# Optimization experiments

Hardware: AMD Instinct MI355X
Metric: run time of the kernel (lower is better)

The kernel has to match this reference:

```python
import jax, jax.numpy as jnp
import numpy as np

# ---- production-scale dims (see shape_source) ----
B, S = 256, 512            # batch, seq_len
HD, INTD = 512, 256        # hidden_dim, hidden_dim // dim_div
N_TEST, N_ITEM, N_TAG = 1500, 9454, 912
N_USER = 7442
GE_ROWS = N_USER + N_ITEM  # LightGCN table: users + items
N_CONT = 3


def _layer_norm(x, g, b, eps=1e-5):
    mu = jnp.mean(x, axis=-1, keepdims=True)
    var = jnp.var(x, axis=-1, keepdims=True)
    return (x - mu) * jax.lax.rsqrt(var + eps) * g + b


def setup_inputs() -> dict:
    key = jax.random.key(0)
    ks = jax.random.split(key, 14)
    f = lambda k, shp, s=0.02: jax.random.normal(k, shp, dtype=jnp.float32) * s
    return {
        # forward data args
        "cate_testId": jax.random.randint(ks[0], (B, S), 0, N_TEST),
        "cate_itemId": jax.random.randint(ks[1], (B, S), 0, N_ITEM),
        "cate_tag": jax.random.randint(ks[2], (B, S), 0, N_TAG),
        "cont_feats": jax.random.normal(ks[3], (B, S, N_CONT), dtype=jnp.float32),
        "interaction": jax.random.randint(ks[4], (B, S), 0, 3),
        # learned parameters
        "emb_interaction": f(ks[5], (3, INTD)),
        "emb_testId": f(ks[6], (N_TEST + 1, INTD)),
        "emb_itemId": f(ks[7], (N_ITEM + 1, INTD)),
        "emb_tag": f(ks[8], (N_TAG + 1, INTD)),
        "graph_table": f(ks[9], (GE_ROWS, HD)),           # pre-trained LightGCN embedding (np.load in torch)
        "graph_W": f(ks[10], (HD, INTD), 0.05),            # graph_linear (in, out) layout
        "graph_b": jnp.zeros((INTD,), jnp.float32),
        "comb_W": f(ks[11], (INTD * 5, HD // 2)),          # intd*(3 cate + 1 graph + interaction)
        "comb_b": jnp.zeros((HD // 2,), jnp.float32),
        "comb_g": jnp.ones((HD // 2,), jnp.float32),
        "comb_beta": jnp.zeros((HD // 2,), jnp.float32),
        "cont_W": f(ks[12], (N_CONT, HD // 2), 0.1),
        "cont_b": jnp.zeros((HD // 2,), jnp.float32),
        "cont_g": jnp.ones((HD // 2,), jnp.float32),
        "cont_beta": jnp.zeros((HD // 2,), jnp.float32),
    }


def reference(cate_testId, cate_itemId, cate_tag, cont_feats, interaction,
              emb_interaction, emb_testId, emb_itemId, emb_tag,
              graph_table, graph_W, graph_b,
              comb_W, comb_b, comb_g, comb_beta,
              cont_W, cont_b, cont_g, cont_beta):
    # categorical + interaction embedding lookups: [B,S,INTD] each
    e_int = emb_interaction[interaction]
    e_test = emb_testId[cate_testId]
    e_item = emb_itemId[cate_itemId]
    e_tag = emb_tag[cate_tag]
    # graph embedding path: fused gather (replaces the CPU python-loop gather)
    # indexes row (n_userID - 1 + value) of the LightGCN table, value from data[0]=testId
    g = graph_table[N_USER - 1 + cate_testId]          # [B,S,HD]
    g = g @ graph_W + graph_b                          # [B,S,INTD]
    embed = jnp.concatenate([e_int, e_test, e_item, e_tag, g], axis=-1)  # [B,S,5*INTD]
    cate = _layer_norm(embed @ comb_W + comb_b, comb_g, comb_beta)       # [B,S,HD//2]
    cont = _layer_norm(cont_feats @ cont_W + cont_b, cont_g, cont_beta)  # [B,S,HD//2]
    return jnp.concatenate([cate, cont], axis=-1)                        # [B,S,HD]
```

## Files before the change

### kernel.cpp

```cpp
#include <hip/hip_runtime.h>
#include <hip/hip_bf16.h>

#define NTOK   (256 * 512)
#define N_USER 7442

using bf16 = __hip_bfloat16;
typedef float f32x4 __attribute__((ext_vector_type(4)));

static __device__ __forceinline__ float4 ld4(const float* p) {
    return *reinterpret_cast<const float4*>(p);
}
static __device__ __forceinline__ float bfl(unsigned u) {
    union { unsigned u; float f; } c; c.u = u << 16; return c.f;
}
static __device__ __forceinline__ float bfh(unsigned u) {
    union { unsigned u; float f; } c; c.u = u & 0xFFFF0000u; return c.f;
}
static __device__ __forceinline__ void st_nt4(float* p, float x, float y, float z, float w) {
    f32x4 v; v.x = x; v.y = y; v.z = z; v.w = w;
    __builtin_nontemporal_store(v, reinterpret_cast<f32x4*>(p));
}
static __device__ __forceinline__ float rnd_bf(float x) {
    return __bfloat162float(__float2bfloat16(x));
}
static __device__ __forceinline__ void st_bf4(bf16* dst, float4 v) {
    union { bf16 h[4]; uint2 u; } pk;
    pk.h[0] = __float2bfloat16(v.x);
    pk.h[1] = __float2bfloat16(v.y);
    pk.h[2] = __float2bfloat16(v.z);
    pk.h[3] = __float2bfloat16(v.w);
    *reinterpret_cast<uint2*>(dst) = pk.u;
}

template <int CTRL, int ROW_MASK>
static __device__ __forceinline__ float dpp_add(float x) {
    const int sh = __builtin_amdgcn_update_dpp(0, __float_as_int(x), CTRL, ROW_MASK, 0xf, true);
    return x + __int_as_float(sh);
}
static __device__ __forceinline__ float wave_sum(float x) {
    x = dpp_add<0x111, 0xf>(x);
    x = dpp_add<0x112, 0xf>(x);
    x = dpp_add<0x114, 0xf>(x);
    x = dpp_add<0x118, 0xf>(x);
    x = dpp_add<0x142, 0xa>(x);
    x = dpp_add<0x143, 0xc>(x);
    return __int_as_float(__builtin_amdgcn_readlane(__float_as_int(x), 63));
}
static __device__ __forceinline__ float dot4(float4 a, float4 b) {
    return a.x * b.x + a.y * b.y + a.z * b.z + a.w * b.w;
}

#define RG  8
#define RSP 16
#define NB_TESTG 188
#define NB_ITEM  591
#define NB_TAG   58
#define NB_INT   1
#define NB_PC    (NB_TESTG + NB_ITEM + NB_TAG + NB_INT)
#define NB_CONT  2048
#define NB_A     (NB_PC + NB_CONT)

__global__ __launch_bounds__(256) void precompute_cont_kernel(
    const float* __restrict__ emb_int,  const float* __restrict__ emb_test,
    const float* __restrict__ emb_item, const float* __restrict__ emb_tag,
    const float* __restrict__ graph_tab, const float* __restrict__ graph_W,
    const float* __restrict__ graph_b,
    const float* __restrict__ comb_W,   const float* __restrict__ comb_b,
    const float* __restrict__ cont_feats,
    const float* __restrict__ cont_W,   const float* __restrict__ cont_b,
    const float* __restrict__ cont_g,   const float* __restrict__ cont_beta,
    bf16* __restrict__ Pint, bf16* __restrict__ Ptestg,
    bf16* __restrict__ Pitem, bf16* __restrict__ Ptag,
    float* __restrict__ Rint, float* __restrict__ Rtestg,
    float* __restrict__ Ritem, float* __restrict__ Rtag,
    float* __restrict__ out) {
    __shared__ float lds[4096];
    const int tid  = threadIdx.x;
    const int w    = tid >> 6;
    const int lane = tid & 63;
    const int c    = lane * 4;
    const int b    = blockIdx.x;

    if (b >= NB_PC) {
        const float4 w0  = ld4(cont_W + 0 * 256 + c);
        const float4 w1  = ld4(cont_W + 1 * 256 + c);
        const float4 w2  = ld4(cont_W + 2 * 256 + c);
        const float4 cb  = ld4(cont_b + c);
        const float4 g42 = ld4(cont_g + c);
        const float4 b42 = ld4(cont_beta + c);

        const float inv256 = 1.f / 256.f;
        const float M0  = wave_sum(w0.x + w0.y + w0.z + w0.w) * inv256;
        const float M1  = wave_sum(w1.x + w1.y + w1.z + w1.w) * inv256;
        const float M2  = wave_sum(w2.x + w2.y + w2.z + w2.w) * inv256;
        const float M3  = wave_sum(cb.x + cb.y + cb.z + cb.w) * inv256;
        const float P00 = wave_sum(dot4(w0, w0)) * inv256;
        const float P11 = wave_sum(dot4(w1, w1)) * inv256;
        const float P22 = wave_sum(dot4(w2, w2)) * inv256;
        const float P33 = wave_sum(dot4(cb, cb)) * inv256;
        const float P01 = wave_sum(dot4(w0, w1)) * inv256;
        const float P02 = wave_sum(dot4(w0, w2)) * inv256;
        const float P12 = wave_sum(dot4(w1, w2)) * inv256;
        const float P03 = wave_sum(dot4(w0, cb)) * inv256;
        const float P13 = wave_sum(dot4(w1, cb)) * inv256;
        const float P23 = wave_sum(dot4(w2, cb)) * inv256;

        const int wid = (b - NB_PC) * 4 + w;
        const int t0  = wid * 16;
        for (int k4 = 0; k4 < 4; ++k4) {
            const int tb = t0 + k4 * 4;
            const float4 cf0 = ld4(cont_feats + (size_t)tb * 3);
            const float4 cf1 = ld4(cont_feats + (size_t)tb * 3 + 4);
            const float4 cf2 = ld4(cont_feats + (size_t)tb * 3 + 8);
            const float cf[12] = {cf0.x, cf0.y, cf0.z, cf0.w,
                                  cf1.x, cf1.y, cf1.z, cf1.w,
                                  cf2.x, cf2.y, cf2.z, cf2.w};
            #pragma unroll
            for (int j = 0; j < 4; ++j) {
                const int t = tb + j;
                const float c0 = cf[j * 3 + 0];
                const float c1 = cf[j * 3 + 1];
                const float c2 = cf[j * 3 + 2];
                const float mu2 = c0 * M0 + c1 * M1 + c2 * M2 + M3;
                const float e2  = c0 * c0 * P00 + c1 * c1 * P11 + c2 * c2 * P22 + P33
                                + 2.f * (c0 * c1 * P01 + c0 * c2 * P02 + c1 * c2 * P12
                                       + c0 * P03 + c1 * P13 + c2 * P23);
                const float var2 = e2 - mu2 * mu2;
                const float inv2 = rsqrtf(var2 + 1e-5f);

                const float ux = c0 * w0.x + c1 * w1.x + c2 * w2.x + cb.x;
                const float uy = c0 * w0.y + c1 * w1.y + c2 * w2.y + cb.y;
                const float uz = c0 * w0.z + c1 * w1.z + c2 * w2.z + cb.z;
                const float uw = c0 * w0.w + c1 * w1.w + c2 * w2.w + cb.w;

                st_nt4(out + (size_t)t * 512 + 256 + c,
                       (ux - mu2) * inv2 * g42.x + b42.x,
                       (uy - mu2) * inv2 * g42.y + b42.y,
                       (uz - mu2) * inv2 * g42.z + b42.z,
                       (uw - mu2) * inv2 * g42.w + b42.w);
            }
        }
        return;
    }

    const float* W0 = comb_W;
    const float* W1 = comb_W + 256 * 256;
    const float* W2 = comb_W + 512 * 256;
    const float* W3 = comb_W + 768 * 256;
    const float* W4 = comb_W + 1024 * 256;

    if (b < NB_TESTG) {
        const int row0 = b * RG;
        const int nr   = min(RG, 1500 - row0);

        for (int i = tid; i < nr * 512; i += 256) {
            const int r = i >> 9, m = i & 511;
            lds[r * 512 + m] = graph_tab[(size_t)(N_USER - 1 + row0 + r) * 512 + m];
        }
        __syncthreads();

        float4 acc[2];
        acc[0] = float4{0.f, 0.f, 0.f, 0.f};
        acc[1] = float4{0.f, 0.f, 0.f, 0.f};
        for (int m = 0; m < 512; m += 4) {
            const float4 wv0 = ld4(graph_W + (m + 0) * 256 + c);
            const float4 wv1 = ld4(graph_W + (m + 1) * 256 + c);
            const float4 wv2 = ld4(graph_W + (m + 2) * 256 + c);
            const float4 wv3 = ld4(graph_W + (m + 3) * 256 + c);
            #pragma unroll
            for (int r = 0; r < 2; ++r) {
                const int rr = min(w * 2 + r, nr - 1);
                const float4 e = ld4(&lds[rr * 512 + m]);
                acc[r].x += e.x * wv0.x + e.y * wv1.x + e.z * wv2.x + e.w * wv3.x;
                acc[r].y += e.x * wv0.y + e.y * wv1.y + e.z * wv2.y + e.w * wv3.y;
                acc[r].z += e.x * wv0.z + e.y * wv1.z + e.z * wv2.z + e.w * wv3.z;
                acc[r].w += e.x * wv0.w + e.y * wv1.w + e.z * wv2.w + e.w * wv3.w;
            }
        }
        __syncthreads();

        #pragma unroll
        for (int r = 0; r < 2; ++r)
            *reinterpret_cast<float4*>(&lds[(w * 2 + r) * 256 + c]) = acc[r];
        for (int i = tid; i < nr * 256; i += 256) {
            const int r = i >> 8, m = i & 255;
            lds[2048 + r * 256 + m] = emb_test[(size_t)(row0 + r) * 256 + m];
        }
        __syncthreads();

        float4 acc2[2];
        float4 bacc = float4{0.f, 0.f, 0.f, 0.f};
        acc2[0] = float4{0.f, 0.f, 0.f, 0.f};
        acc2[1] = float4{0.f, 0.f, 0.f, 0.f};
        for (int m = 0; m < 256; m += 4) {
            const float4 w40 = ld4(W4 + (m + 0) * 256 + c);
            const float4 w41 = ld4(W4 + (m + 1) * 256 + c);
            const float4 w42 = ld4(W4 + (m + 2) * 256 + c);
            const float4 w43 = ld4(W4 + (m + 3) * 256 + c);
            const float4 w10 = ld4(W1 + (m + 0) * 256 + c);
            const float4 w11 = ld4(W1 + (m + 1) * 256 + c);
            const float4 w12 = ld4(W1 + (m + 2) * 256 + c);
            const float4 w13 = ld4(W1 + (m + 3) * 256 + c);
            const float gb0 = graph_b[m + 0], gb1 = graph_b[m + 1];
            const float gb2 = graph_b[m + 2], gb3 = graph_b[m + 3];
            bacc.x += gb0 * w40.x + gb1 * w41.x + gb2 * w42.x + gb3 * w43.x;
            bacc.y += gb0 * w40.y + gb1 * w41.y + gb2 * w42.y + gb3 * w43.y;
            bacc.z += gb0 * w40.z + gb1 * w41.z + gb2 * w42.z + gb3 * w43.z;
            bacc.w += gb0 * w40.w + gb1 * w41.w + gb2 * w42.w + gb3 * w43.w;
            #pragma unroll
            for (int r = 0; r < 2; ++r) {
                const int rr = min(w * 2 + r, nr - 1);
                const float4 tv = ld4(&lds[rr * 256 + m]);
                const float4 ev = ld4(&lds[2048 + rr * 256 + m]);
                acc2[r].x += tv.x * w40.x + tv.y * w41.x + tv.z * w42.x + tv.w * w43.x
                           + ev.x * w10.x + ev.y * w11.x + ev.z * w12.x + ev.w * w13.x;
                acc2[r].y += tv.x * w40.y + tv.y * w41.y + tv.z * w42.y + tv.w * w43.y
                           + ev.x * w10.y + ev.y * w11.y + ev.z * w12.y + ev.w * w13.y;
                acc2[r].z += tv.x * w40.z + tv.y * w41.z + tv.z * w42.z + tv.w * w43.z
                           + ev.x * w10.z + ev.y * w11.z + ev.z * w12.z + ev.w * w13.z;
                acc2[r].w += tv.x * w40.w + tv.y * w41.w + tv.z * w42.w + tv.w * w43.w
                           + ev.x * w10.w + ev.y * w11.w + ev.z * w12.w + ev.w * w13.w;
            }
        }
        const float4 cbv = ld4(comb_b + c);
        #pragma unroll
        for (int r = 0; r < 2; ++r) {
            const int row = w * 2 + r;
            float4 o;
            o.x = acc2[r].x + bacc.x + cbv.x;
            o.y = acc2[r].y + bacc.y + cbv.y;
            o.z = acc2[r].z + bacc.z + cbv.z;
            o.w = acc2[r].w + bacc.w + cbv.w;
            const float rs = wave_sum(rnd_bf(o.x) + rnd_bf(o.y) + rnd_bf(o.z) + rnd_bf(o.w));
            if (row < nr) {
                st_bf4(Ptestg + (size_t)(row0 + row) * 256 + c, o);
                if (lane == 0) Rtestg[row0 + row] = rs;
            }
        }
    } else {
        const float* E; const float* W; bf16* P; float* R; int row0, Rn;
        const int sb = b - NB_TESTG;
        if (sb < NB_ITEM)               { E = emb_item; W = W2; P = Pitem; R = Ritem; row0 = sb * RSP;             Rn = 9455; }
        else if (sb < NB_ITEM + NB_TAG) { E = emb_tag;  W = W3; P = Ptag;  R = Rtag;  row0 = (sb - NB_ITEM) * RSP; Rn = 913;  }
        else                            { E = emb_int;  W = W0; P = Pint;  R = Rint;  row0 = 0;                    Rn = 3;    }
        const int nr = min(RSP, Rn - row0);

        for (int i = tid; i < nr * 256; i += 256) {
            const int r = i >> 8, m = i & 255;
            lds[r * 256 + m] = E[(size_t)(row0 + r) * 256 + m];
        }
        __syncthreads();

        if (w * 4 < nr) {
            float4 acc[4];
            #pragma unroll
            for (int r = 0; r < 4; ++r) acc[r] = float4{0.f, 0.f, 0.f, 0.f};
            for (int m = 0; m < 256; m += 4) {
                const float4 wv0 = ld4(W + (m + 0) * 256 + c);
                const float4 wv1 = ld4(W + (m + 1) * 256 + c);
                const float4 wv2 = ld4(W + (m + 2) * 256 + c);
                const float4 wv3 = ld4(W + (m + 3) * 256 + c);
                #pragma unroll
                for (int r = 0; r < 4; ++r) {
                    const int rr = min(w * 4 + r, nr - 1);
                    const float4 e = ld4(&lds[rr * 256 + m]);
                    acc[r].x += e.x * wv0.x + e.y * wv1.x + e.z * wv2.x + e.w * wv3.x;
                    acc[r].y += e.x * wv0.y + e.y * wv1.y + e.z * wv2.y + e.w * wv3.y;
                    acc[r].z += e.x * wv0.z + e.y * wv1.z + e.z * wv2.z + e.w * wv3.z;
                    acc[r].w += e.x * wv0.w + e.y * wv1.w + e.z * wv2.w + e.w * wv3.w;
                }
            }
            #pragma unroll
            for (int r = 0; r < 4; ++r) {
                const int row = w * 4 + r;
                const float rs = wave_sum(rnd_bf(acc[r].x) + rnd_bf(acc[r].y) +
                                          rnd_bf(acc[r].z) + rnd_bf(acc[r].w));
                if (row < nr) {
                    st_bf4(P + (size_t)(row0 + row) * 256 + c, acc[r]);
                    if (lane == 0) R[row0 + row] = rs;
                }
            }
        }
    }
}

__global__ __launch_bounds__(256) void main_cate_kernel(
    const int* __restrict__ testId, const int* __restrict__ itemId,
    const int* __restrict__ tagId,  const int* __restrict__ inter,
    const bf16* __restrict__ Pint, const bf16* __restrict__ Ptestg,
    const bf16* __restrict__ Pitem, const bf16* __restrict__ Ptag,
    const float* __restrict__ Rint, const float* __restrict__ Rtestg,
    const float* __restrict__ Ritem, const float* __restrict__ Rtag,
    const float* __restrict__ comb_g, const float* __restrict__ comb_beta,
    float* __restrict__ out) {
    const int wid  = blockIdx.x * 4 + (threadIdx.x >> 6);
    const int lane = threadIdx.x & 63;
    const int c    = lane * 4;

    const float4 g4 = ld4(comb_g + c);
    const float4 b4 = ld4(comb_beta + c);
    const uint2 p0 = *reinterpret_cast<const uint2*>(Pint + 0 * 256 + c);
    const uint2 p1 = *reinterpret_cast<const uint2*>(Pint + 1 * 256 + c);
    const uint2 p2 = *reinterpret_cast<const uint2*>(Pint + 2 * 256 + c);
    const float ri0 = Rint[0], ri1 = Rint[1], ri2 = Rint[2];

    const int tb = wid * 4;
    const int4 tiv = *reinterpret_cast<const int4*>(testId + tb);
    const int4 iiv = *reinterpret_cast<const int4*>(itemId + tb);
    const int4 tgv = *reinterpret_cast<const int4*>(tagId  + tb);
    const int4 ivv = *reinterpret_cast<const int4*>(inter  + tb);
    const int tis[4] = {tiv.x, tiv.y, tiv.z, tiv.w};
    const int iis[4] = {iiv.x, iiv.y, iiv.z, iiv.w};
    const int tgs[4] = {tgv.x, tgv.y, tgv.z, tgv.w};
    const int ivs[4] = {ivv.x, ivv.y, ivv.z, ivv.w};

    uint2 gT[4], gI[4], gG[4];
    float sT[4], sI[4], sG[4];
    #pragma unroll
    for (int j = 0; j < 4; ++j) {
        gT[j] = *reinterpret_cast<const uint2*>(Ptestg + (size_t)tis[j] * 256 + c);
        gI[j] = *reinterpret_cast<const uint2*>(Pitem  + (size_t)iis[j] * 256 + c);
        gG[j] = *reinterpret_cast<const uint2*>(Ptag   + (size_t)tgs[j] * 256 + c);
        sT[j] = Rtestg[tis[j]];
        sI[j] = Ritem[iis[j]];
        sG[j] = Rtag[tgs[j]];
    }

    #pragma unroll
    for (int j = 0; j < 4; ++j) {
        const int t = tb + j;

        uint2 u0;
        u0.x = ivs[j] == 0 ? p0.x : (ivs[j] == 1 ? p1.x : p2.x);
        u0.y = ivs[j] == 0 ? p0.y : (ivs[j] == 1 ? p1.y : p2.y);
        const float sInt = ivs[j] == 0 ? ri0 : (ivs[j] == 1 ? ri1 : ri2);

        const float vx = bfl(u0.x) + bfl(gT[j].x) + bfl(gI[j].x) + bfl(gG[j].x);
        const float vy = bfh(u0.x) + bfh(gT[j].x) + bfh(gI[j].x) + bfh(gG[j].x);
        const float vz = bfl(u0.y) + bfl(gT[j].y) + bfl(gI[j].y) + bfl(gG[j].y);
        const float vw = bfh(u0.y) + bfh(gT[j].y) + bfh(gI[j].y) + bfh(gG[j].y);

        const float s   = sInt + sT[j] + sI[j] + sG[j];
        const float ss  = wave_sum(vx * vx + vy * vy + vz * vz + vw * vw);
        const float mu  = s * (1.f / 256.f);
        const float var = ss * (1.f / 256.f) - mu * mu;
        const float inv = rsqrtf(var + 1e-5f);

        st_nt4(out + (size_t)t * 512 + c,
               (vx - mu) * inv * g4.x + b4.x,
               (vy - mu) * inv * g4.y + b4.y,
               (vz - mu) * inv * g4.z + b4.z,
               (vw - mu) * inv * g4.w + b4.w);
    }
}

extern "C" void kernel_launch(void* const* d_in, const int* in_sizes, int n_in,
                              void* d_out, int out_size, void* d_ws, size_t ws_size,
                              hipStream_t stream) {
    const int*   testId     = (const int*)d_in[0];
    const int*   itemId     = (const int*)d_in[1];
    const int*   tagId      = (const int*)d_in[2];
    const float* cont_feats = (const float*)d_in[3];
    const int*   inter      = (const int*)d_in[4];
    const float* emb_int    = (const float*)d_in[5];
    const float* emb_test   = (const float*)d_in[6];
    const float* emb_item   = (const float*)d_in[7];
    const float* emb_tag    = (const float*)d_in[8];
    const float* graph_tab  = (const float*)d_in[9];
    const float* graph_W    = (const float*)d_in[10];
    const float* graph_b    = (const float*)d_in[11];
    const float* comb_W     = (const float*)d_in[12];
    const float* comb_b     = (const float*)d_in[13];
    const float* comb_g     = (const float*)d_in[14];
    const float* comb_beta  = (const float*)d_in[15];
    const float* cont_W     = (const float*)d_in[16];
    const float* cont_b     = (const float*)d_in[17];
    const float* cont_g     = (const float*)d_in[18];
    const float* cont_beta  = (const float*)d_in[19];
    float* out              = (float*)d_out;

    bf16* ws     = (bf16*)d_ws;
    bf16* Pitem  = ws;
    bf16* Ptestg = Pitem  + 9455 * 256;
    bf16* Ptag   = Ptestg + 1500 * 256;
    bf16* Pint   = Ptag   +  913 * 256;
    float* Ritem  = (float*)(Pint + 3 * 256);
    float* Rtestg = Ritem  + 9455;
    float* Rtag   = Rtestg + 1500;
    float* Rint   = Rtag   +  913;

    precompute_cont_kernel<<<NB_A, 256, 0, stream>>>(
        emb_int, emb_test, emb_item, emb_tag, graph_tab, graph_W, graph_b,
        comb_W, comb_b, cont_feats, cont_W, cont_b, cont_g, cont_beta,
        Pint, Ptestg, Pitem, Ptag,
        Rint, Rtestg, Ritem, Rtag, out);

    main_cate_kernel<<<NTOK / (4 * 4), 256, 0, stream>>>(
        testId, itemId, tagId, inter,
        Pint, Ptestg, Pitem, Ptag,
        Rint, Rtestg, Ritem, Rtag,
        comb_g, comb_beta, out);
}
```

Baseline: 109.9 us.

## Split precompute GEMV K-dimension across two waves with 128-thread blocks

Shrinks the precompute/cont kernel to 128-thread blocks (two waves) and doubles the number of cont blocks to keep the same token coverage. In the table-projection blocks, each wave now handles all rows but only half of the reduction dimension, and the partial sums are combined through LDS. The aim is to load each weight row once per block for all rows instead of once per wave, cutting redundant global weight traffic. The cost is more accumulator registers (up to 16 float4), extra LDS reduction passes and barriers, and a larger LDS footprint.

```diff
diff --git a/kernel.cpp b/kernel.cpp
--- a/kernel.cpp
+++ b/kernel.cpp
@@ -50,17 +50,15 @@
     return a.x * b.x + a.y * b.y + a.z * b.z + a.w * b.w;
 }
 
-#define RG  8
-#define RSP 16
 #define NB_TESTG 188
 #define NB_ITEM  591
 #define NB_TAG   58
 #define NB_INT   1
 #define NB_PC    (NB_TESTG + NB_ITEM + NB_TAG + NB_INT)
-#define NB_CONT  2048
+#define NB_CONT  4096
 #define NB_A     (NB_PC + NB_CONT)
 
-__global__ __launch_bounds__(256) void precompute_cont_kernel(
+__global__ __launch_bounds__(128) void precompute_cont_kernel(
     const float* __restrict__ emb_int,  const float* __restrict__ emb_test,
     const float* __restrict__ emb_item, const float* __restrict__ emb_tag,
     const float* __restrict__ graph_tab, const float* __restrict__ graph_W,
@@ -74,7 +72,7 @@
     float* __restrict__ Rint, float* __restrict__ Rtestg,
     float* __restrict__ Ritem, float* __restrict__ Rtag,
     float* __restrict__ out) {
-    __shared__ float lds[4096];
+    __shared__ float lds[6400];
     const int tid  = threadIdx.x;
     const int w    = tid >> 6;
     const int lane = tid & 63;
@@ -105,7 +103,7 @@
         const float P13 = wave_sum(dot4(w1, cb)) * inv256;
         const float P23 = wave_sum(dot4(w2, cb)) * inv256;
 
-        const int wid = (b - NB_PC) * 4 + w;
+        const int wid = (b - NB_PC) * 2 + w;
         const int t0  = wid * 16;
         for (int k4 = 0; k4 < 4; ++k4) {
             const int tb = t0 + k4 * 4;
@@ -125,8 +123,7 @@
                 const float e2  = c0 * c0 * P00 + c1 * c1 * P11 + c2 * c2 * P22 + P33
                                 + 2.f * (c0 * c1 * P01 + c0 * c2 * P02 + c1 * c2 * P12
                                        + c0 * P03 + c1 * P13 + c2 * P23);
-                const float var2 = e2 - mu2 * mu2;
-                const float inv2 = rsqrtf(var2 + 1e-5f);
+                const float inv2 = rsqrtf(e2 - mu2 * mu2 + 1e-5f);
 
                 const float ux = c0 * w0.x + c1 * w1.x + c2 * w2.x + cb.x;
                 const float uy = c0 * w0.y + c1 * w1.y + c2 * w2.y + cb.y;
@@ -150,27 +147,28 @@
     const float* W4 = comb_W + 1024 * 256;
 
     if (b < NB_TESTG) {
-        const int row0 = b * RG;
-        const int nr   = min(RG, 1500 - row0);
-
-        for (int i = tid; i < nr * 512; i += 256) {
-            const int r = i >> 9, m = i & 511;
-            lds[r * 512 + m] = graph_tab[(size_t)(N_USER - 1 + row0 + r) * 512 + m];
-        }
-        __syncthreads();
-
-        float4 acc[2];
-        acc[0] = float4{0.f, 0.f, 0.f, 0.f};
-        acc[1] = float4{0.f, 0.f, 0.f, 0.f};
-        for (int m = 0; m < 512; m += 4) {
+        const int row0 = b * 8;
+        const int nr   = min(8, 1500 - row0);
+
+        for (int i = tid; i < 1024; i += 128) {
+            const int r = i >> 7, m4 = (i & 127) * 4;
+            const int rr = min(r, nr - 1);
+            *reinterpret_cast<float4*>(&lds[r * 512 + m4]) =
+                ld4(graph_tab + (size_t)(N_USER - 1 + row0 + rr) * 512 + m4);
+        }
+        __syncthreads();
+
+        float4 acc[8];
+        #pragma unroll
+        for (int r = 0; r < 8; ++r) acc[r] = float4{0.f, 0.f, 0.f, 0.f};
+        for (int m = w * 256; m < w * 256 + 256; m += 4) {
             const float4 wv0 = ld4(graph_W + (m + 0) * 256 + c);
             const float4 wv1 = ld4(graph_W + (m + 1) * 256 + c);
             const float4 wv2 = ld4(graph_W + (m + 2) * 256 + c);
             const float4 wv3 = ld4(graph_W + (m + 3) * 256 + c);
             #pragma unroll
-            for (int r = 0; r < 2; ++r) {
-                const int rr = min(w * 2 + r, nr - 1);
-                const float4 e = ld4(&lds[rr * 512 + m]);
+            for (int r = 0; r < 8; ++r) {
+                const float4 e = ld4(&lds[r * 512 + m]);
                 acc[r].x += e.x * wv0.x + e.y * wv1.x + e.z * wv2.x + e.w * wv3.x;
                 acc[r].y += e.x * wv0.y + e.y * wv1.y + e.z * wv2.y + e.w * wv3.y;
                 acc[r].z += e.x * wv0.z + e.y * wv1.z + e.z * wv2.z + e.w * wv3.z;
@@ -179,20 +177,33 @@
         }
         __syncthreads();
 
+        if (w == 0) {
+            #pragma unroll
+            for (int r = 0; r < 8; ++r)
+                *reinterpret_cast<float4*>(&lds[4096 + r * 256 + c]) = acc[r];
+        }
+        __syncthreads();
+        if (w == 1) {
+            #pragma unroll
+            for (int r = 0; r < 8; ++r) {
+                float4 t = ld4(&lds[4096 + r * 256 + c]);
+                t.x += acc[r].x; t.y += acc[r].y; t.z += acc[r].z; t.w += acc[r].w;
+                *reinterpret_cast<float4*>(&lds[4096 + r * 256 + c]) = t;
+            }
+        }
+        for (int i = tid; i < 512; i += 128) {
+            const int r = i >> 6, m4 = (i & 63) * 4;
+            const int rr = min(r, nr - 1);
+            *reinterpret_cast<float4*>(&lds[r * 256 + m4]) =
+                ld4(emb_test + (size_t)(row0 + rr) * 256 + m4);
+        }
+        __syncthreads();
+
+        float4 acc2[8];
+        float4 bacc = float4{0.f, 0.f, 0.f, 0.f};
         #pragma unroll
-        for (int r = 0; r < 2; ++r)
-            *reinterpret_cast<float4*>(&lds[(w * 2 + r) * 256 + c]) = acc[r];
-        for (int i = tid; i < nr * 256; i += 256) {
-            const int r = i >> 8, m = i & 255;
-            lds[2048 + r * 256 + m] = emb_test[(size_t)(row0 + r) * 256 + m];
-        }
-        __syncthreads();
-
-        float4 acc2[2];
-        float4 bacc = float4{0.f, 0.f, 0.f, 0.f};
-        acc2[0] = float4{0.f, 0.f, 0.f, 0.f};
-        acc2[1] = float4{0.f, 0.f, 0.f, 0.f};
-        for (int m = 0; m < 256; m += 4) {
+        for (int r = 0; r < 8; ++r) acc2[r] = float4{0.f, 0.f, 0.f, 0.f};
+        for (int m = w * 128; m < w * 128 + 128; m += 4) {
             const float4 w40 = ld4(W4 + (m + 0) * 256 + c);
             const float4 w41 = ld4(W4 + (m + 1) * 256 + c);
             const float4 w42 = ld4(W4 + (m + 2) * 256 + c);
@@ -208,10 +219,9 @@
             bacc.z += gb0 * w40.z + gb1 * w41.z + gb2 * w42.z + gb3 * w43.z;
             bacc.w += gb0 * w40.w + gb1 * w41.w + gb2 * w42.w + gb3 * w43.w;
             #pragma unroll
-            for (int r = 0; r < 2; ++r) {
-                const int rr = min(w * 2 + r, nr - 1);
-                const float4 tv = ld4(&lds[rr * 256 + m]);
-                const float4 ev = ld4(&lds[2048 + rr * 256 + m]);
+            for (int r = 0; r < 8; ++r) {
+                const float4 tv = ld4(&lds[4096 + r * 256 + m]);
+                const float4 ev = ld4(&lds[r * 256 + m]);
                 acc2[r].x += tv.x * w40.x + tv.y * w41.x + tv.z * w42.x + tv.w * w43.x
                            + ev.x * w10.x + ev.y * w11.x + ev.z * w12.x + ev.w * w13.x;
                 acc2[r].y += tv.x * w40.y + tv.y * w41.y + tv.z * w42.y + tv.w * w43.y
@@ -222,63 +232,101 @@
                            + ev.x * w10.w + ev.y * w11.w + ev.z * w12.w + ev.w * w13.w;
             }
         }
+        if (w == 0) {
+            #pragma unroll
+            for (int r = 0; r < 8; ++r)
+                *reinterpret_cast<float4*>(&lds[2048 + r * 256 + c]) = acc2[r];
+            *reinterpret_cast<float4*>(&lds[6144 + c]) = bacc;
+        }
+        __syncthreads();
+        if (w == 1) {
+            #pragma unroll
+            for (int r = 0; r < 8; ++r) {
+                float4 t = ld4(&lds[2048 + r * 256 + c]);
+                t.x += acc2[r].x; t.y += acc2[r].y; t.z += acc2[r].z; t.w += acc2[r].w;
+                *reinterpret_cast<float4*>(&lds[2048 + r * 256 + c]) = t;
+            }
+            float4 t = ld4(&lds[6144 + c]);
+            t.x += bacc.x; t.y += bacc.y; t.z += bacc.z; t.w += bacc.w;
+            *reinterpret_cast<float4*>(&lds[6144 + c]) = t;
+        }
+        __syncthreads();
+
         const float4 cbv = ld4(comb_b + c);
+        const float4 bb  = ld4(&lds[6144 + c]);
         #pragma unroll
-        for (int r = 0; r < 2; ++r) {
-            const int row = w * 2 + r;
-            float4 o;
-            o.x = acc2[r].x + bacc.x + cbv.x;
-            o.y = acc2[r].y + bacc.y + cbv.y;
-            o.z = acc2[r].z + bacc.z + cbv.z;
-            o.w = acc2[r].w + bacc.w + cbv.w;
+        for (int r4 = 0; r4 < 4; ++r4) {
+            const int r = w * 4 + r4;
+            float4 o = ld4(&lds[2048 + r * 256 + c]);
+            o.x += bb.x + cbv.x;
+            o.y += bb.y + cbv.y;
+            o.z += bb.z + cbv.z;
+            o.w += bb.w + cbv.w;
             const float rs = wave_sum(rnd_bf(o.x) + rnd_bf(o.y) + rnd_bf(o.z) + rnd_bf(o.w));
-            if (row < nr) {
-                st_bf4(Ptestg + (size_t)(row0 + row) * 256 + c, o);
-                if (lane == 0) Rtestg[row0 + row] = rs;
+            if (r < nr) {
+                st_bf4(Ptestg + (size_t)(row0 + r) * 256 + c, o);
+                if (lane == 0) Rtestg[row0 + r] = rs;
             }
         }
     } else {
         const float* E; const float* W; bf16* P; float* R; int row0, Rn;
         const int sb = b - NB_TESTG;
-        if (sb < NB_ITEM)               { E = emb_item; W = W2; P = Pitem; R = Ritem; row0 = sb * RSP;             Rn = 9455; }
-        else if (sb < NB_ITEM + NB_TAG) { E = emb_tag;  W = W3; P = Ptag;  R = Rtag;  row0 = (sb - NB_ITEM) * RSP; Rn = 913;  }
-        else                            { E = emb_int;  W = W0; P = Pint;  R = Rint;  row0 = 0;                    Rn = 3;    }
-        const int nr = min(RSP, Rn - row0);
-
-        for (int i = tid; i < nr * 256; i += 256) {
-            const int r = i >> 8, m = i & 255;
-            lds[r * 256 + m] = E[(size_t)(row0 + r) * 256 + m];
-        }
-        __syncthreads();
-
-        if (w * 4 < nr) {
-            float4 acc[4];
-            #pragma unroll
-            for (int r = 0; r < 4; ++r) acc[r] = float4{0.f, 0.f, 0.f, 0.f};
-            for (int m = 0; m < 256; m += 4) {
-                const float4 wv0 = ld4(W + (m + 0) * 256 + c);
-                const float4 wv1 = ld4(W + (m + 1) * 256 + c);
-                const float4 wv2 = ld4(W + (m + 2) * 256 + c);
-                const float4 wv3 = ld4(W + (m + 3) * 256 + c);
-                #pragma unroll
-                for (int r = 0; r < 4; ++r) {
-                    const int rr = min(w * 4 + r, nr - 1);
-                    const float4 e = ld4(&lds[rr * 256 + m]);
-                    acc[r].x += e.x * wv0.x + e.y * wv1.x + e.z * wv2.x + e.w * wv3.x;
-                    acc[r].y += e.x * wv0.y + e.y * wv1.y + e.z * wv2.y + e.w * wv3.y;
-                    acc[r].z += e.x * wv0.z + e.y * wv1.z + e.z * wv2.z + e.w * wv3.z;
-                    acc[r].w += e.x * wv0.w + e.y * wv1.w + e.z * wv2.w + e.w * wv3.w;
-                }
-            }
-            #pragma unroll
-            for (int r = 0; r < 4; ++r) {
-                const int row = w * 4 + r;
-                const float rs = wave_sum(rnd_bf(acc[r].x) + rnd_bf(acc[r].y) +
-                                          rnd_bf(acc[r].z) + rnd_bf(acc[r].w));
-                if (row < nr) {
-                    st_bf4(P + (size_t)(row0 + row) * 256 + c, acc[r]);
-                    if (lane == 0) R[row0 + row] = rs;
-                }
+        if (sb < NB_ITEM)               { E = emb_item; W = W2; P = Pitem; R = Ritem; row0 = sb * 16;             Rn = 9455; }
+        else if (sb < NB_ITEM + NB_TAG) { E = emb_tag;  W = W3; P = Ptag;  R = Rtag;  row0 = (sb - NB_ITEM) * 16; Rn = 913;  }
+        else                            { E = emb_int;  W = W0; P = Pint;  R = Rint;  row0 = 0;                   Rn = 3;    }
+        const int nr = min(16, Rn - row0);
+
+        for (int i = tid; i < 1024; i += 128) {
+            const int r = i >> 6, m4 = (i & 63) * 4;
+            const int rr = min(r, nr - 1);
+            *reinterpret_cast<float4*>(&lds[r * 256 + m4]) =
+                ld4(E + (size_t)(row0 + rr) * 256 + m4);
+        }
+        __syncthreads();
+
+        float4 acc[16];
+        #pragma unroll
+        for (int r = 0; r < 16; ++r) acc[r] = float4{0.f, 0.f, 0.f, 0.f};
+        for (int m = w * 128; m < w * 128 + 128; m += 4) {
+            const float4 wv0 = ld4(W + (m + 0) * 256 + c);
+            const float4 wv1 = ld4(W + (m + 1) * 256 + c);
+            const float4 wv2 = ld4(W + (m + 2) * 256 + c);
+            const float4 wv3 = ld4(W + (m + 3) * 256 + c);
+            #pragma unroll
+            for (int r = 0; r < 16; ++r) {
+                const float4 e = ld4(&lds[r * 256 + m]);
+                acc[r].x += e.x * wv0.x + e.y * wv1.x + e.z * wv2.x + e.w * wv3.x;
+                acc[r].y += e.x * wv0.y + e.y * wv1.y + e.z * wv2.y + e.w * wv3.y;
+                acc[r].z += e.x * wv0.z + e.y * wv1.z + e.z * wv2.z + e.w * wv3.z;
+                acc[r].w += e.x * wv0.w + e.y * wv1.w + e.z * wv2.w + e.w * wv3.w;
+            }
+        }
+        __syncthreads();
+
+        if (w == 0) {
+            #pragma unroll
+            for (int r = 0; r < 16; ++r)
+                *reinterpret_cast<float4*>(&lds[r * 256 + c]) = acc[r];
+        }
+        __syncthreads();
+        if (w == 1) {
+            #pragma unroll
+            for (int r = 0; r < 16; ++r) {
+                float4 t = ld4(&lds[r * 256 + c]);
+                t.x += acc[r].x; t.y += acc[r].y; t.z += acc[r].z; t.w += acc[r].w;
+                *reinterpret_cast<float4*>(&lds[r * 256 + c]) = t;
+            }
+        }
+        __syncthreads();
+
+        #pragma unroll
+        for (int r8 = 0; r8 < 8; ++r8) {
+            const int r = w * 8 + r8;
+            const float4 o = ld4(&lds[r * 256 + c]);
+            const float rs = wave_sum(rnd_bf(o.x) + rnd_bf(o.y) + rnd_bf(o.z) + rnd_bf(o.w));
+            if (r < nr) {
+                st_bf4(P + (size_t)(row0 + r) * 256 + c, o);
+                if (lane == 0) R[row0 + r] = rs;
             }
         }
     }
@@ -389,7 +437,7 @@
     float* Rtag   = Rtestg + 1500;
     float* Rint   = Rtag   +  913;
 
-    precompute_cont_kernel<<<NB_A, 256, 0, stream>>>(
+    precompute_cont_kernel<<<NB_A, 128, 0, stream>>>(
         emb_int, emb_test, emb_item, emb_tag, graph_tab, graph_W, graph_b,
         comb_W, comb_b, cont_feats, cont_W, cont_b, cont_g, cont_beta,
         Pint, Ptestg, Pitem, Ptag,
```

Result: faster. 104.1 us (median of 2 runs) (-5.3%).
